# Performance work log

Hardware: AMD Instinct MI355X
Metric: run time of the kernel (lower is better)

Reference implementation:

```python
import jax, jax.numpy as jnp
import numpy as np

CONF_THRES = 0.25
IOU_THRES = 0.45
MAX_DET = 1000
MAX_WH = 4096.0  # class offset used by YOLOv5 for class-aware NMS
K = 1024         # fixed candidate count (static-shape stand-in for conf filtering)


def xywh2xyxy(b):
    cx, cy, w, h = b[..., 0], b[..., 1], b[..., 2], b[..., 3]
    return jnp.stack([cx - w / 2, cy - h / 2, cx + w / 2, cy + h / 2], axis=-1)


def pairwise_iou(boxes):
    # boxes: [K,4] xyxy -> [K,K] IoU
    x1, y1, x2, y2 = boxes[:, 0], boxes[:, 1], boxes[:, 2], boxes[:, 3]
    area = (x2 - x1) * (y2 - y1)
    ix1 = jnp.maximum(x1[:, None], x1[None, :])
    iy1 = jnp.maximum(y1[:, None], y1[None, :])
    ix2 = jnp.minimum(x2[:, None], x2[None, :])
    iy2 = jnp.minimum(y2[:, None], y2[None, :])
    inter = jnp.clip(ix2 - ix1, 0.0) * jnp.clip(iy2 - iy1, 0.0)
    return inter / (area[:, None] + area[None, :] - inter + 1e-9)


def nms_image(pred):
    # pred: [N, 5+nc] = xywh, obj, class scores
    boxes = xywh2xyxy(pred[:, :4])                 # [N,4]
    scores = pred[:, 5:] * pred[:, 4:5]            # conf = obj * cls
    conf = jnp.max(scores, axis=-1)                # [N]
    cls = jnp.argmax(scores, axis=-1)              # [N] int
    masked = jnp.where(conf > CONF_THRES, conf, -1.0)
    top_conf, idx = jax.lax.top_k(masked, K)       # sorted desc
    cand_boxes = boxes[idx]                        # [K,4]
    cand_cls = cls[idx]                            # [K]
    cand_valid = top_conf > 0.0                    # below-threshold slots are -1
    # class-aware NMS: offset boxes per class so different classes never overlap
    off_boxes = cand_boxes + (cand_cls.astype(pred.dtype) * MAX_WH)[:, None]
    iou = pairwise_iou(off_boxes)                  # [K,K]

    def step(suppressed, i):
        keep_i = jnp.logical_and(jnp.logical_not(suppressed[i]), cand_valid[i])
        suppressed = jnp.where(keep_i, jnp.logical_or(suppressed, iou[i] > IOU_THRES), suppressed)
        return suppressed, keep_i

    _, keep = jax.lax.scan(step, jnp.zeros((K,), dtype=bool), jnp.arange(K))
    sel_score = jnp.where(keep, top_conf, -1.0)
    fin_score, fin_idx = jax.lax.top_k(sel_score, MAX_DET)
    ok = fin_score > 0.0
    det = jnp.concatenate(
        [cand_boxes[fin_idx],
         top_conf[fin_idx][:, None],
         cand_cls[fin_idx].astype(pred.dtype)[:, None]],
        axis=-1,
    )  # [MAX_DET, 6] = x1,y1,x2,y2,conf,cls
    return jnp.where(ok[:, None], det, 0.0)


def setup_inputs() -> dict:
    key = jax.random.key(0)
    k1, k2, k3, k4 = jax.random.split(key, 4)
    B, N, NC = 16, 25200, 80
    cxcy = jax.random.uniform(k1, (B, N, 2), dtype=jnp.float32) * 640.0
    wh = jax.random.uniform(k2, (B, N, 2), dtype=jnp.float32) * 96.0 + 4.0
    obj = jax.random.uniform(k3, (B, N, 1), dtype=jnp.float32)
    cls = jax.random.uniform(k4, (B, N, NC), dtype=jnp.float32)
    pred = jnp.concatenate([cxcy, wh, obj, cls], axis=-1)
    return {"pred": pred}


def reference(pred):
    # [B, MAX_DET, 6] zero-padded detections per image
    return jax.vmap(nms_image)(pred)
```

## Files before the change

### kernel.cpp

```cpp
#include <hip/hip_runtime.h>
#include <stdint.h>

typedef unsigned int u32;
typedef unsigned long long u64;

#define BB 16
#define NN 25200
#define ROWLEN 85
#define KCAND 1024
#define MAXDET 1000
#define CONF_T 0.25f
#define IOU_T 0.45f
#define MAX_WH 4096.0f
#define KBASE 0xBE800000u
#define NBLK 394

__device__ __forceinline__ u32 f2key(float f) {
  u32 u = __float_as_uint(f);
  return (u & 0x80000000u) ? ~u : (u | 0x80000000u);
}
__device__ __forceinline__ float key2f(u32 k) {
  u32 u = (k & 0x80000000u) ? (k & 0x7FFFFFFFu) : ~k;
  return __uint_as_float(u);
}

__global__ __launch_bounds__(64) void k_score(const float* __restrict__ pred,
                                              u32* __restrict__ keys,
                                              int* __restrict__ clsArr) {
  __shared__ float sh[64 * ROWLEN];
  const int t = threadIdx.x;
  const int bi = blockIdx.x;
  const int img = blockIdx.y;
  const int r0 = bi * 64;
  const float4* src = (const float4*)(pred + ((size_t)img * NN + r0) * ROWLEN);
  float4* dst = (float4*)sh;
  if (r0 + 64 <= NN) {
    #pragma unroll
    for (int i = 0; i < 21; ++i) dst[t + 64 * i] = src[t + 64 * i];
    if (t < 16) dst[t + 64 * 21] = src[t + 64 * 21];
  } else {
    const int nf4 = (NN - r0) * ROWLEN / 4;
    for (int i = t; i < nf4; i += 64) dst[i] = src[i];
  }
  __syncthreads();
  const int nrows = (r0 + 64 <= NN) ? 64 : (NN - r0);
  if (t < nrows) {
    const float* row = sh + t * ROWLEN;
    float obj = row[4];
    float v0 = -INFINITY, v1 = -INFINITY, v2 = -INFINITY, v3 = -INFINITY;
    int j0 = 0, j1 = 20, j2 = 40, j3 = 60;
    #pragma unroll
    for (int c = 0; c < 20; ++c) {
      float s0 = obj * row[5 + c];
      float s1 = obj * row[25 + c];
      float s2 = obj * row[45 + c];
      float s3 = obj * row[65 + c];
      if (s0 > v0) { v0 = s0; j0 = c; }
      if (s1 > v1) { v1 = s1; j1 = 20 + c; }
      if (s2 > v2) { v2 = s2; j2 = 40 + c; }
      if (s3 > v3) { v3 = s3; j3 = 60 + c; }
    }
    float v = v0; int j = j0;
    if (v1 > v) { v = v1; j = j1; }
    if (v2 > v) { v = v2; j = j2; }
    if (v3 > v) { v = v3; j = j3; }
    u32 key = (v > CONF_T) ? (f2key(v) - KBASE) : 0u;
    size_t r = (size_t)img * NN + r0 + t;
    keys[r] = key;
    clsArr[r] = j;
  }
}

__device__ __forceinline__ void bt_apply(u64& e, u64 p, int m, int j, int k) {
  bool lower = ((m & j) == 0);
  bool dir = ((m & k) == 0);
  bool takeMax = (lower == dir);
  u64 mx = e > p ? e : p;
  u64 mn = e > p ? p : e;
  e = takeMax ? mx : mn;
}

__global__ __launch_bounds__(1024, 4) void k_select(const float* __restrict__ pred,
                                                    const u32* __restrict__ keys,
                                                    const int* __restrict__ clsArr,
                                                    float* __restrict__ candScore,
                                                    float* __restrict__ candBox,
                                                    int* __restrict__ candCls) {
  __shared__ u32 hist[16][257];
  __shared__ u32 hist1[257];
  __shared__ u64 buf[2048];
  __shared__ u32 sh_sel, sh_rem, sh_cnt;
  const int b = blockIdx.x;
  const int tid = threadIdx.x;
  const int lane = tid & 63;
  const int wv = tid >> 6;
  const u32* kk = keys + (size_t)b * NN;
  u32* histflat = (u32*)hist;

  u32 rr[25];
  #pragma unroll
  for (int it = 0; it < 25; ++it) {
    int n0 = tid + it * 1024;
    rr[it] = (n0 < NN) ? kk[n0] : 0u;
  }

  for (int i = tid; i < 16 * 257; i += 1024) histflat[i] = 0;
  if (tid == 0) sh_cnt = 0;
  __syncthreads();
  #pragma unroll
  for (int it = 0; it < 25; ++it) {
    u32 r = rr[it];
    if (r != 0u) atomicAdd(&hist[wv][r >> 16], 1u);
  }
  __syncthreads();
  if (wv == 0) {
    u32 c0 = 0, c1 = 0, c2 = 0, c3 = 0;
    #pragma unroll
    for (int w = 0; w < 16; ++w) {
      c0 += hist[w][4 * lane + 0];
      c1 += hist[w][4 * lane + 1];
      c2 += hist[w][4 * lane + 2];
      c3 += hist[w][4 * lane + 3];
    }
    u32 tl = c0 + c1 + c2 + c3;
    u32 incl = tl;
    #pragma unroll
    for (int off = 1; off <= 32; off <<= 1) {
      u32 o = __shfl_down(incl, off, 64);
      if (lane + off < 64) incl += o;
    }
    u32 S0 = incl;
    u32 S1 = S0 - c0;
    u32 S2 = S1 - c1;
    u32 S3 = S2 - c2;
    u32 S4 = S3 - c3;
    u32 rem = KCAND;
    if (S0 >= rem && S1 < rem) { sh_sel = 4 * lane + 0; sh_rem = rem - S1; }
    if (S1 >= rem && S2 < rem) { sh_sel = 4 * lane + 1; sh_rem = rem - S2; }
    if (S2 >= rem && S3 < rem) { sh_sel = 4 * lane + 2; sh_rem = rem - S3; }
    if (S3 >= rem && S4 < rem) { sh_sel = 4 * lane + 3; sh_rem = rem - S4; }
  }
  __syncthreads();
  u32 prefix = (sh_sel << 16);
  u32 remaining = sh_rem;
  u32 himask = 0xFF0000u;
  __syncthreads();

  #pragma unroll
  for (int pass = 1; pass < 3; ++pass) {
    const int shift = 16 - 8 * pass;
    if (tid < 256) hist1[tid] = 0u;
    __syncthreads();
    #pragma unroll
    for (int it = 0; it < 25; ++it) {
      u32 r = rr[it];
      if (r != 0u && (r & himask) == prefix)
        atomicAdd(&hist1[(r >> shift) & 255], 1u);
    }
    __syncthreads();
    if (wv == 0) {
      const int j4 = lane << 2;
      u32 c0 = hist1[j4 + 0], c1 = hist1[j4 + 1], c2 = hist1[j4 + 2], c3 = hist1[j4 + 3];
      u32 tl = c0 + c1 + c2 + c3;
      u32 incl = tl;
      #pragma unroll
      for (int off = 1; off <= 32; off <<= 1) {
        u32 o = __shfl_down(incl, off, 64);
        if (lane + off < 64) incl += o;
      }
      u32 S0 = incl;
      u32 S1 = S0 - c0;
      u32 S2 = S1 - c1;
      u32 S3 = S2 - c2;
      u32 S4 = S3 - c3;
      u32 rem = remaining;
      if (S0 >= rem && S1 < rem) { sh_sel = 4 * lane + 0; sh_rem = rem - S1; }
      if (S1 >= rem && S2 < rem) { sh_sel = 4 * lane + 1; sh_rem = rem - S2; }
      if (S2 >= rem && S3 < rem) { sh_sel = 4 * lane + 2; sh_rem = rem - S3; }
      if (S3 >= rem && S4 < rem) { sh_sel = 4 * lane + 3; sh_rem = rem - S4; }
    }
    __syncthreads();
    prefix |= (sh_sel << shift);
    remaining = sh_rem;
    himask |= (0xFFu << shift);
    __syncthreads();
  }
  const u32 T = prefix;

  #pragma unroll
  for (int it = 0; it < 25; ++it) {
    int n0 = tid + it * 1024;
    u32 r = rr[it];
    bool match = (r >= T);
    u64 bal = __ballot(match);
    if (bal) {
      int leader = __ffsll((unsigned long long)bal) - 1;
      u32 base = 0;
      u32 cnt = (u32)__popcll(bal);
      if (lane == leader) base = atomicAdd(&sh_cnt, cnt);
      base = __shfl(base, leader, 64);
      if (match) {
        u32 pos = base + (u32)__popcll(bal & ((1ull << lane) - 1ull));
        if (pos < 2048) buf[pos] = ((u64)r << 32) | (u32)(~(u32)n0);
      }
    }
  }
  __syncthreads();
  u32 c = sh_cnt; if (c > 2048) c = 2048;
  for (int t = tid; t < 2048; t += 1024) if (t >= (int)c) buf[t] = 0;
  __syncthreads();

  u64 e0 = buf[tid];
  if (c <= 1024) {
    #pragma unroll
    for (int k = 2; k <= 64; k <<= 1) {
      #pragma unroll
      for (int j = k >> 1; j > 0; j >>= 1) {
        u64 p0 = __shfl_xor(e0, j, 64);
        bt_apply(e0, p0, tid, j, k);
      }
    }
    for (int k = 128; k <= 1024; k <<= 1) {
      for (int j = k >> 1; j >= 64; j >>= 1) {
        buf[tid] = e0;
        __syncthreads();
        u64 p0 = buf[tid ^ j];
        bt_apply(e0, p0, tid, j, k);
        __syncthreads();
      }
      #pragma unroll
      for (int j = 32; j > 0; j >>= 1) {
        u64 p0 = __shfl_xor(e0, j, 64);
        bt_apply(e0, p0, tid, j, k);
      }
    }
  } else {
    u64 e1 = buf[tid + 1024];
    #pragma unroll
    for (int k = 2; k <= 64; k <<= 1) {
      #pragma unroll
      for (int j = k >> 1; j > 0; j >>= 1) {
        u64 p0 = __shfl_xor(e0, j, 64);
        u64 p1 = __shfl_xor(e1, j, 64);
        bt_apply(e0, p0, tid, j, k);
        bt_apply(e1, p1, tid + 1024, j, k);
      }
    }
    for (int k = 128; k <= 2048; k <<= 1) {
      int jstart = k >> 1;
      if (k == 2048) {
        u64 mx = e0 > e1 ? e0 : e1;
        u64 mn = e0 > e1 ? e1 : e0;
        e0 = mx; e1 = mn;
        jstart = 512;
      }
      for (int j = jstart; j >= 64; j >>= 1) {
        buf[tid] = e0; buf[tid + 1024] = e1;
        __syncthreads();
        u64 p0 = buf[tid ^ j];
        u64 p1 = buf[(tid ^ j) + 1024];
        bt_apply(e0, p0, tid, j, k);
        bt_apply(e1, p1, tid + 1024, j, k);
        __syncthreads();
      }
      #pragma unroll
      for (int j = 32; j > 0; j >>= 1) {
        u64 p0 = __shfl_xor(e0, j, 64);
        u64 p1 = __shfl_xor(e1, j, 64);
        bt_apply(e0, p0, tid, j, k);
        bt_apply(e1, p1, tid + 1024, j, k);
      }
    }
  }
  {
    u64 e = e0;
    u32 r = (u32)(e >> 32);
    u32 idx = ~(u32)e;
    if (idx >= NN) idx = 0;
    float sc = key2f(r + KBASE);
    size_t g = (size_t)b * KCAND + tid;
    candScore[g] = sc;
    const float* p = pred + ((size_t)b * NN + idx) * ROWLEN;
    float cx = p[0], cy = p[1], w = p[2], h = p[3];
    float4 bx;
    bx.x = cx - 0.5f * w;
    bx.y = cy - 0.5f * h;
    bx.z = cx + 0.5f * w;
    bx.w = cy + 0.5f * h;
    ((float4*)candBox)[g] = bx;
    candCls[g] = clsArr[(size_t)b * NN + idx];
  }
}

__global__ __launch_bounds__(64) void k_iou(const float* __restrict__ candBox,
                                            const int* __restrict__ candCls,
                                            u64* __restrict__ matT) {
  #pragma clang fp contract(off)
  __shared__ float4 sb[64];
  __shared__ float sa[64];
  const int rc = blockIdx.x;
  const int cc = blockIdx.y;
  const int b  = blockIdx.z;
  if (rc > cc) return;
  const int lane = threadIdx.x;
  {
    int rrow = rc * 64 + lane;
    float4 bx = ((const float4*)candBox)[(size_t)b * KCAND + rrow];
    float off = (float)candCls[(size_t)b * KCAND + rrow] * MAX_WH;
    float x1 = bx.x + off, y1 = bx.y + off, x2 = bx.z + off, y2 = bx.w + off;
    float4 sbv; sbv.x = x1; sbv.y = y1; sbv.z = x2; sbv.w = y2;
    sb[lane] = sbv;
    sa[lane] = (x2 - x1) * (y2 - y1);
  }
  int col = cc * 64 + lane;
  float4 cb = ((const float4*)candBox)[(size_t)b * KCAND + col];
  float coff = (float)candCls[(size_t)b * KCAND + col] * MAX_WH;
  float cx1 = cb.x + coff, cy1 = cb.y + coff, cx2 = cb.z + coff, cy2 = cb.w + coff;
  float car = (cx2 - cx1) * (cy2 - cy1);
  __syncthreads();
  u64 myw = 0;
  for (int r = 0; r < 64; ++r) {
    float4 rb = sb[r];
    float ra = sa[r];
    float ix1 = fmaxf(rb.x, cx1);
    float iy1 = fmaxf(rb.y, cy1);
    float ix2 = fminf(rb.z, cx2);
    float iy2 = fminf(rb.w, cy2);
    float dx = fmaxf(ix2 - ix1, 0.0f);
    float dy = fmaxf(iy2 - iy1, 0.0f);
    float inter = dx * dy;
    float den = ra + car;
    den = den - inter;
    den = den + 1e-9f;
    float iou = inter / den;
    u64 bal = __ballot(iou > IOU_T);
    if (lane == r) myw = bal;
  }
  matT[(((size_t)b * 16 + cc) << 10) + rc * 64 + lane] = myw;
}

#define TRIDX(c, cp) (((c) * ((c)-1)) / 2 + (cp))
__global__ __launch_bounds__(256, 1) void k_scan_out(const u64* __restrict__ matT,
                                                     const float* __restrict__ candScore,
                                                     const float* __restrict__ candBox,
                                                     const int* __restrict__ candCls,
                                                     float* __restrict__ out) {
  __shared__ u64 sTri[120 * 64];
  __shared__ u64 sKeep[16];
  const int b = blockIdx.x;
  const int tid = threadIdx.x;
  const u64* Mb = matT + ((size_t)b << 14);

  #pragma unroll
  for (int c = 1; c < 16; ++c) {
    const u64* src = Mb + ((size_t)c << 10);
    u64* dst = sTri + (size_t)TRIDX(c, 0) * 64;
    #pragma unroll
    for (int i = 0; i < c * 64; i += 256) {
      int idx = i + tid;
      if (idx < c * 64) dst[idx] = src[idx];
    }
  }
  __syncthreads();

  if (tid < 64) {
    const int lane = tid;
    u64 vw[16], dg[16], kcw[16];
    #pragma unroll
    for (int w = 0; w < 16; ++w) {
      float sc = candScore[(size_t)b * KCAND + w * 64 + lane];
      vw[w] = __ballot(sc > 0.0f);
    }
    #pragma unroll
    for (int c = 0; c < 16; ++c)
      dg[c] = Mb[((size_t)c << 10) + c * 64 + lane];

    #pragma unroll
    for (int c = 0; c < 16; ++c) {
      u64 acc = 0;
      #pragma unroll
      for (int cp = 0; cp < 15; ++cp) {
        if (cp < c) {
          if ((kcw[cp] >> lane) & 1ull) acc |= sTri[(size_t)TRIDX(c, cp) * 64 + lane];
        }
      }
      #pragma unroll
      for (int st = 1; st < 64; st <<= 1) acc |= __shfl_xor(acc, st, 64);
      u64 d = dg[c];
      u64 s = acc;
      u64 kc = 0;
      u64 vc = vw[c];
      #pragma unroll
      for (int g = 0; g < 8; ++g) {
        u64 dgp[8];
        #pragma unroll
        for (int j = 0; j < 8; ++j) dgp[j] = __shfl(d, g * 8 + j, 64);
        #pragma unroll
        for (int j = 0; j < 8; ++j) {
          int i = g * 8 + j;
          bool ok = !((s >> i) & 1ull) && ((vc >> i) & 1ull);
          if (ok) { s |= dgp[j]; kc |= (1ull << i); }
        }
      }
      kcw[c] = kc;
    }
    if (lane < 16) sKeep[lane] = kcw[lane];
  }
  __syncthreads();

  int total = 0;
  #pragma unroll
  for (int w = 0; w < 16; ++w) total += __popcll(sKeep[w]);
  int kept_eff = total < MAXDET ? total : MAXDET;
  float* outb = out + (size_t)b * MAXDET * 6;
  #pragma unroll
  for (int rr2 = 0; rr2 < 4; ++rr2) {
    const int t = tid + rr2 * 256;
    u64 word = sKeep[t >> 6];
    int bit = (int)((word >> (t & 63)) & 1ull);
    int rank = 0;
    for (int w = 0; w < (t >> 6); ++w) rank += __popcll(sKeep[w]);
    rank += __popcll(word & ((1ull << (t & 63)) - 1ull));
    if (bit && rank < MAXDET) {
      size_t g = (size_t)b * KCAND + t;
      float4 bx = ((const float4*)candBox)[g];
      float sc = candScore[g];
      float cf = (float)candCls[g];
      float* o = outb + (size_t)rank * 6;
      o[0] = bx.x; o[1] = bx.y; o[2] = bx.z; o[3] = bx.w; o[4] = sc; o[5] = cf;
    }
    if (t < MAXDET && t >= kept_eff) {
      float* o = outb + (size_t)t * 6;
      o[0] = 0.f; o[1] = 0.f; o[2] = 0.f; o[3] = 0.f; o[4] = 0.f; o[5] = 0.f;
    }
  }
}

extern "C" void kernel_launch(void* const* d_in, const int* in_sizes, int n_in,
                              void* d_out, int out_size, void* d_ws, size_t ws_size,
                              hipStream_t stream) {
  const float* pred = (const float*)d_in[0];
  float* out = (float*)d_out;
  char* ws = (char*)d_ws;
  size_t o = 0;
  u32*   keysW     = (u32*)  (ws + o); o += (size_t)BB * NN * 4;
  int*   clsArr    = (int*)  (ws + o); o += (size_t)BB * NN * 4;
  float* candScore = (float*)(ws + o); o += (size_t)BB * KCAND * 4;
  float* candBox   = (float*)(ws + o); o += (size_t)BB * KCAND * 16;
  int*   candCls   = (int*)  (ws + o); o += (size_t)BB * KCAND * 4;
  o = (o + 255) & ~(size_t)255;
  u64*   matT      = (u64*)  (ws + o); o += (size_t)BB * KCAND * 16 * 8;

  k_score<<<dim3(NBLK, BB), 64, 0, stream>>>(pred, keysW, clsArr);
  k_select<<<BB, 1024, 0, stream>>>(pred, keysW, clsArr, candScore, candBox, candCls);
  k_iou<<<dim3(16, 16, BB), 64, 0, stream>>>(candBox, candCls, matT);
  k_scan_out<<<BB, 256, 0, stream>>>(matT, candScore, candBox, candCls, out);
}
```

Measured before the change: 293.4 us.

## Fuse pairwise IoU bitmask computation into candidate selection kernel

```diff
diff --git a/kernel.cpp b/kernel.cpp
--- a/kernel.cpp
+++ b/kernel.cpp
@@ -80,15 +80,54 @@
   e = takeMax ? mx : mn;
 }
 
+__device__ __forceinline__ void wedge_pairs(const float4* __restrict__ sOff,
+                                            const float* __restrict__ sAr,
+                                            u64* __restrict__ matT,
+                                            int b, int wv, int lane) {
+  #pragma clang fp contract(off)
+  for (int p = wv; p < 136; p += 16) {
+    int base = 0, cc = 0;
+    while (p >= base + cc + 1) { base += cc + 1; ++cc; }
+    int rc = p - base;
+    int col = cc * 64 + lane;
+    float4 cb = sOff[col];
+    float cx1 = cb.x, cy1 = cb.y, cx2 = cb.z, cy2 = cb.w;
+    float car = sAr[col];
+    u64 myw = 0;
+    for (int r = 0; r < 64; ++r) {
+      int rowi = rc * 64 + r;
+      float4 rb = sOff[rowi];
+      float ra = sAr[rowi];
+      float ix1 = fmaxf(rb.x, cx1);
+      float iy1 = fmaxf(rb.y, cy1);
+      float ix2 = fminf(rb.z, cx2);
+      float iy2 = fminf(rb.w, cy2);
+      float dx = fmaxf(ix2 - ix1, 0.0f);
+      float dy = fmaxf(iy2 - iy1, 0.0f);
+      float inter = dx * dy;
+      float den = ra + car;
+      den = den - inter;
+      den = den + 1e-9f;
+      float iou = inter / den;
+      u64 bal = __ballot(iou > IOU_T);
+      if (lane == r) myw = bal;
+    }
+    matT[(((size_t)b * 16 + cc) << 10) + rc * 64 + lane] = myw;
+  }
+}
+
 __global__ __launch_bounds__(1024, 4) void k_select(const float* __restrict__ pred,
                                                     const u32* __restrict__ keys,
                                                     const int* __restrict__ clsArr,
                                                     float* __restrict__ candScore,
                                                     float* __restrict__ candBox,
-                                                    int* __restrict__ candCls) {
+                                                    int* __restrict__ candCls,
+                                                    u64* __restrict__ matT) {
   __shared__ u32 hist[16][257];
   __shared__ u32 hist1[257];
   __shared__ u64 buf[2048];
+  __shared__ float4 sOff[KCAND];
+  __shared__ float sAr[KCAND];
   __shared__ u32 sh_sel, sh_rem, sh_cnt;
   const int b = blockIdx.x;
   const int tid = threadIdx.x;
@@ -288,55 +327,16 @@
     bx.z = cx + 0.5f * w;
     bx.w = cy + 0.5f * h;
     ((float4*)candBox)[g] = bx;
-    candCls[g] = clsArr[(size_t)b * NN + idx];
-  }
-}
-
-__global__ __launch_bounds__(64) void k_iou(const float* __restrict__ candBox,
-                                            const int* __restrict__ candCls,
-                                            u64* __restrict__ matT) {
-  #pragma clang fp contract(off)
-  __shared__ float4 sb[64];
-  __shared__ float sa[64];
-  const int rc = blockIdx.x;
-  const int cc = blockIdx.y;
-  const int b  = blockIdx.z;
-  if (rc > cc) return;
-  const int lane = threadIdx.x;
-  {
-    int rrow = rc * 64 + lane;
-    float4 bx = ((const float4*)candBox)[(size_t)b * KCAND + rrow];
-    float off = (float)candCls[(size_t)b * KCAND + rrow] * MAX_WH;
-    float x1 = bx.x + off, y1 = bx.y + off, x2 = bx.z + off, y2 = bx.w + off;
-    float4 sbv; sbv.x = x1; sbv.y = y1; sbv.z = x2; sbv.w = y2;
-    sb[lane] = sbv;
-    sa[lane] = (x2 - x1) * (y2 - y1);
-  }
-  int col = cc * 64 + lane;
-  float4 cb = ((const float4*)candBox)[(size_t)b * KCAND + col];
-  float coff = (float)candCls[(size_t)b * KCAND + col] * MAX_WH;
-  float cx1 = cb.x + coff, cy1 = cb.y + coff, cx2 = cb.z + coff, cy2 = cb.w + coff;
-  float car = (cx2 - cx1) * (cy2 - cy1);
-  __syncthreads();
-  u64 myw = 0;
-  for (int r = 0; r < 64; ++r) {
-    float4 rb = sb[r];
-    float ra = sa[r];
-    float ix1 = fmaxf(rb.x, cx1);
-    float iy1 = fmaxf(rb.y, cy1);
-    float ix2 = fminf(rb.z, cx2);
-    float iy2 = fminf(rb.w, cy2);
-    float dx = fmaxf(ix2 - ix1, 0.0f);
-    float dy = fmaxf(iy2 - iy1, 0.0f);
-    float inter = dx * dy;
-    float den = ra + car;
-    den = den - inter;
-    den = den + 1e-9f;
-    float iou = inter / den;
-    u64 bal = __ballot(iou > IOU_T);
-    if (lane == r) myw = bal;
-  }
-  matT[(((size_t)b * 16 + cc) << 10) + rc * 64 + lane] = myw;
+    int cls = clsArr[(size_t)b * NN + idx];
+    candCls[g] = cls;
+    float off = (float)cls * MAX_WH;
+    float4 ob;
+    ob.x = bx.x + off; ob.y = bx.y + off; ob.z = bx.z + off; ob.w = bx.w + off;
+    sOff[tid] = ob;
+    sAr[tid] = (ob.z - ob.x) * (ob.w - ob.y);
+  }
+  __syncthreads();
+  wedge_pairs(sOff, sAr, matT, b, wv, lane);
 }
 
 #define TRIDX(c, cp) (((c) * ((c)-1)) / 2 + (cp))
@@ -452,7 +452,6 @@
   u64*   matT      = (u64*)  (ws + o); o += (size_t)BB * KCAND * 16 * 8;
 
   k_score<<<dim3(NBLK, BB), 64, 0, stream>>>(pred, keysW, clsArr);
-  k_select<<<BB, 1024, 0, stream>>>(pred, keysW, clsArr, candScore, candBox, candCls);
-  k_iou<<<dim3(16, 16, BB), 64, 0, stream>>>(candBox, candCls, matT);
+  k_select<<<BB, 1024, 0, stream>>>(pred, keysW, clsArr, candScore, candBox, candCls, matT);
   k_scan_out<<<BB, 256, 0, stream>>>(matT, candScore, candBox, candCls, out);
 }
```

Measured after the change: 391.8 us. 33.5% more time.
